# Kernel tuning notes

Hardware: AMD Instinct MI355X
Metric: run time of the kernel (lower is better)

Reference implementation:

```python
import jax, jax.numpy as jnp
import numpy as np

NUM_HEADS = 3
DIM = 96
MLP_HIDDEN = int(DIM * 4.0)
LN_EPS = 1e-5


def _layernorm(x, g, b):
    mu = jnp.mean(x, axis=-1, keepdims=True)
    var = jnp.mean(jnp.square(x - mu), axis=-1, keepdims=True)
    return (x - mu) * jax.lax.rsqrt(var + LN_EPS) * g + b


def setup_inputs() -> dict:
    key = jax.random.key(0)
    ks = jax.random.split(key, 12)
    B, H, W, T, C = 1, 48, 48, 48, DIM
    L = H * W * T
    s = 0.02
    return {
        "x": jax.random.normal(ks[0], (B, L, C), dtype=jnp.float32),
        "mask_matrix": jnp.zeros((1, 1), dtype=jnp.float32),
        "ln1_g": jnp.ones((C,), jnp.float32),
        "ln1_b": jnp.zeros((C,), jnp.float32),
        "qkv_w": jax.random.normal(ks[1], (3 * C, C), jnp.float32) * s,
        "qkv_b": jnp.zeros((3 * C,), jnp.float32),
        "proj_w": jax.random.normal(ks[2], (C, C), jnp.float32) * s,
        "proj_b": jnp.zeros((C,), jnp.float32),
        "ln2_g": jnp.ones((C,), jnp.float32),
        "ln2_b": jnp.zeros((C,), jnp.float32),
        "fc1_w": jax.random.normal(ks[3], (MLP_HIDDEN, C), jnp.float32) * s,
        "fc1_b": jnp.zeros((MLP_HIDDEN,), jnp.float32),
        "fc2_w": jax.random.normal(ks[4], (C, MLP_HIDDEN), jnp.float32) * s,
        "fc2_b": jnp.zeros((C,), jnp.float32),
        "H": 48, "W": 48, "T": 48,
    }


def reference(x, mask_matrix, ln1_g, ln1_b, qkv_w, qkv_b, proj_w, proj_b,
              ln2_g, ln2_b, fc1_w, fc1_b, fc2_w, fc2_b, H, W, T):
    B, L, C = x.shape
    nh = NUM_HEADS
    hd = C // nh
    scale = hd ** -0.5

    shortcut = x
    h = _layernorm(x, ln1_g, ln1_b)
    # [B,H,W,T,C] -> permute(0,3,1,2,4) -> [B*T, H*W, C]  (axial_dims='12', extra_dim=3)
    h = h.reshape(B, H, W, T, C).transpose(0, 3, 1, 2, 4).reshape(B * T, H * W, C)
    B_, N, _ = h.shape

    qkv = h @ qkv_w.T + qkv_b                       # [B_, N, 3C]
    # faithful to torch: permute(1,0,2) -> reshape(1,N,3,nh,B_*hd) -> permute(2,0,3,1,4)
    qkv = jnp.transpose(qkv, (1, 0, 2)).reshape(1, N, 3, nh, B_ * hd)
    qkv = jnp.transpose(qkv, (2, 0, 3, 1, 4))       # [3, 1, nh, N, B_*hd]
    q, k, v = qkv[0] * scale, qkv[1], qkv[2]

    attn = jax.nn.softmax(q @ jnp.swapaxes(k, -2, -1), axis=-1)  # [1, nh, N, N]
    o = attn @ v                                    # [1, nh, N, B_*hd]
    o = jnp.transpose(o, (0, 2, 1, 3)).reshape(B_, N, C)
    o = o @ proj_w.T + proj_b
    # faithful to torch: plain view back to [B, H*W*T, C] (no inverse permute)
    o = o.reshape(B, H * W * T, C)

    x = shortcut + o
    h2 = _layernorm(x, ln2_g, ln2_b)
    m = jax.nn.gelu(h2 @ fc1_w.T + fc1_b, approximate=False) @ fc2_w.T + fc2_b
    return x + m
```

## Files before the change

kernel.cpp:

```cpp
#include <hip/hip_runtime.h>
#include <hip/hip_bf16.h>
#include <math.h>

typedef __bf16 bf16_t;
typedef __bf16 bf16x8 __attribute__((ext_vector_type(8)));
typedef __bf16 bf16x4 __attribute__((ext_vector_type(4)));
typedef float f32x4 __attribute__((ext_vector_type(4)));

#define AS1q __attribute__((address_space(1)))
#define AS3q __attribute__((address_space(3)))

__device__ __forceinline__ void gload_lds16(const bf16_t* g, bf16_t* l) {
    __builtin_amdgcn_global_load_lds((AS1q void*)g, (AS3q void*)l, 16, 0, 0);
}

#define LROWS   110592
#define CDIM    96
#define NTOK    2304
#define FDIM    1536
#define YSTR    3538944ll
#define SSTR    5308416ll
#define SCALE_Q 0.1767766952966369f

__global__ __launch_bounds__(256)
void conv_w(const float* __restrict__ a, const float* __restrict__ b,
            const float* __restrict__ c, const float* __restrict__ d,
            bf16_t* __restrict__ out)
{
    int i = blockIdx.x * 256 + threadIdx.x;
    float v;
    if (i < 27648)       v = a[i];
    else if (i < 36864)  v = b[i - 27648];
    else if (i < 73728)  v = c[i - 36864];
    else                 v = d[i - 73728];
    out[i] = (bf16_t)v;
}

__global__ __launch_bounds__(256)
void ln4_kernel(const float* __restrict__ x, const float* __restrict__ gamma,
                const float* __restrict__ beta, bf16_t* __restrict__ out, int permute)
{
    int wave = threadIdx.x >> 6;
    int half = (threadIdx.x >> 5) & 1;
    int cl   = threadIdx.x & 31;
    int row  = blockIdx.x * 8 + wave * 2 + half;
    bool act = cl < 24;
    const f32x4* xr = (const f32x4*)(x + (size_t)row * CDIM);
    f32x4 v = {0.f, 0.f, 0.f, 0.f};
    if (act) v = xr[cl];
    float s = v[0] + v[1] + v[2] + v[3];
    #pragma unroll
    for (int off = 16; off > 0; off >>= 1) s += __shfl_xor(s, off, 64);
    float mean = s * (1.f / 96.f);
    f32x4 d = {0.f, 0.f, 0.f, 0.f};
    if (act) { d[0]=v[0]-mean; d[1]=v[1]-mean; d[2]=v[2]-mean; d[3]=v[3]-mean; }
    float vs = d[0]*d[0] + d[1]*d[1] + d[2]*d[2] + d[3]*d[3];
    #pragma unroll
    for (int off = 16; off > 0; off >>= 1) vs += __shfl_xor(vs, off, 64);
    float rstd = rsqrtf(vs * (1.f / 96.f) + 1e-5f);
    size_t orow = row;
    if (permute) { int t = row % 48; int n = row / 48; orow = (size_t)t * NTOK + n; }
    if (act) {
        f32x4 g = ((const f32x4*)gamma)[cl];
        f32x4 b = ((const f32x4*)beta)[cl];
        bf16x4 o;
        #pragma unroll
        for (int j = 0; j < 4; j++) o[j] = (bf16_t)(d[j] * rstd * g[j] + b[j]);
        *(bf16x4*)(out + orow * CDIM + cl * 4) = o;
    }
}

__global__ __launch_bounds__(256)
void transpose_v(const bf16_t* __restrict__ Y, bf16_t* __restrict__ Yv)
{
    __shared__ bf16_t tile[64][65];
    const bf16_t* src = Y + (size_t)(6 + blockIdx.z) * YSTR;
    bf16_t* dst = Yv + (size_t)blockIdx.z * YSTR;
    int m0 = blockIdx.x * 64, n0 = blockIdx.y * 64;
    int nl = threadIdx.x >> 2, ch = threadIdx.x & 3;
    const bf16x8* s8 = (const bf16x8*)(src + (size_t)(n0 + nl) * FDIM + m0 + ch * 16);
    bf16x8 va = s8[0], vb = s8[1];
    #pragma unroll
    for (int j = 0; j < 8; j++) tile[nl][ch * 16 + j] = va[j];
    #pragma unroll
    for (int j = 0; j < 8; j++) tile[nl][ch * 16 + 8 + j] = vb[j];
    __syncthreads();
    bf16_t* d = dst + (size_t)(m0 + nl) * NTOK + n0 + ch * 16;
    #pragma unroll
    for (int j = 0; j < 16; j++) d[j] = tile[ch * 16 + j][nl];
}

__global__ __launch_bounds__(256)
void softmax_k(const float* __restrict__ S, bf16_t* __restrict__ P,
               long long sZ, long long pZ)
{
    __shared__ float red[8];
    const float* sr = S + (size_t)blockIdx.z * sZ + (size_t)blockIdx.x * NTOK;
    bf16_t* pr = P + (size_t)blockIdx.z * pZ + (size_t)blockIdx.x * NTOK;
    int wave = threadIdx.x >> 6, lane = threadIdx.x & 63;
    float v[9];
    float mx = -1e30f;
    #pragma unroll
    for (int t = 0; t < 9; t++) { v[t] = sr[t * 256 + threadIdx.x]; mx = fmaxf(mx, v[t]); }
    for (int off = 32; off > 0; off >>= 1) mx = fmaxf(mx, __shfl_xor(mx, off, 64));
    if (lane == 0) red[wave] = mx;
    __syncthreads();
    mx = fmaxf(fmaxf(red[0], red[1]), fmaxf(red[2], red[3]));
    float sum = 0.f;
    #pragma unroll
    for (int t = 0; t < 9; t++) { v[t] = __expf(v[t] - mx); sum += v[t]; }
    for (int off = 32; off > 0; off >>= 1) sum += __shfl_xor(sum, off, 64);
    if (lane == 0) red[4 + wave] = sum;
    __syncthreads();
    sum = red[4] + red[5] + red[6] + red[7];
    float inv = 1.f / sum;
    #pragma unroll
    for (int t = 0; t < 9; t++) pr[t * 256 + threadIdx.x] = (bf16_t)(v[t] * inv);
}

template<int BN, int EPI, int NBY>
__global__ __launch_bounds__(256, 2)
void gemm_bt(const bf16_t* __restrict__ A, const bf16_t* __restrict__ W,
             void* __restrict__ out, int K,
             long long aZ, long long wZ, long long oZ, float scale)
{
    constexpr int BM = 128, BK = 64;
    constexpr int MI = 4;
    constexpr int NT = BN / 32;
    constexpr int NB = 18 * NBY;
    constexpr int CHK = (NB + 7) / 8;
    __shared__ bf16_t As[BM * BK];
    __shared__ bf16_t Bs[BN * BK];

    int id = blockIdx.x;
    int id2 = (id & 7) * CHK + (id >> 3);
    if (id2 >= NB) return;
    int p  = id2 / 108;
    int r_ = id2 - p * 108;
    int by = p * 6 + (r_ % 6);
    int bx = r_ / 6;

    const int tid = threadIdx.x;
    const int wave = tid >> 6, lane = tid & 63;
    const int quad = lane >> 4, l16 = lane & 15;
    const int wm = wave & 1, wn = wave >> 1;
    const int z = blockIdx.z;
    A += (size_t)z * aZ;
    W += (size_t)z * wZ;
    const int m0 = bx * BM, n0 = by * BN;

    f32x4 acc[MI][NT];
    #pragma unroll
    for (int i = 0; i < MI; i++)
        #pragma unroll
        for (int j = 0; j < NT; j++) { f32x4 zz = {0.f, 0.f, 0.f, 0.f}; acc[i][j] = zz; }

    const int srow = lane >> 3;
    const int scol = lane & 7;

    for (int k0 = 0; k0 < K; k0 += BK) {
        __syncthreads();
        for (int it = wave; it < BM / 8; it += 4) {
            int r = it * 8 + srow;
            int cg = scol ^ (r & 7);
            gload_lds16(A + (size_t)(m0 + r) * K + k0 + cg * 8, &As[it * 512]);
        }
        for (int it = wave; it < BN / 8; it += 4) {
            int r = it * 8 + srow;
            int cg = scol ^ (r & 7);
            gload_lds16(W + (size_t)(n0 + r) * K + k0 + cg * 8, &Bs[it * 512]);
        }
        __syncthreads();

        bf16x8 af[MI][2], bfr[NT][2];
        #pragma unroll
        for (int i = 0; i < MI; i++) {
            int r = wm * 64 + i * 16 + l16;
            #pragma unroll
            for (int kk = 0; kk < 2; kk++)
                af[i][kk] = *(const bf16x8*)&As[r * 64 + (((kk * 4 + quad) ^ (r & 7)) << 3)];
        }
        #pragma unroll
        for (int j = 0; j < NT; j++) {
            int c = wn * (BN / 2) + j * 16 + l16;
            #pragma unroll
            for (int kk = 0; kk < 2; kk++)
                bfr[j][kk] = *(const bf16x8*)&Bs[c * 64 + (((kk * 4 + quad) ^ (c & 7)) << 3)];
        }
        #pragma unroll
        for (int kk = 0; kk < 2; kk++)
            #pragma unroll
            for (int i = 0; i < MI; i++)
                #pragma unroll
                for (int j = 0; j < NT; j++)
                    acc[i][j] = __builtin_amdgcn_mfma_f32_16x16x32_bf16(af[i][kk], bfr[j][kk], acc[i][j], 0, 0, 0);
    }

    #pragma unroll
    for (int i = 0; i < MI; i++)
        #pragma unroll
        for (int j = 0; j < NT; j++)
            #pragma unroll
            for (int ri = 0; ri < 4; ri++) {
                int r = m0 + wm * 64 + i * 16 + quad * 4 + ri;
                int c = n0 + wn * (BN / 2) + j * 16 + l16;
                float v = acc[i][j][ri];
                if constexpr (EPI == 1) {
                    float* op = (float*)out + (size_t)z * oZ;
                    op[(size_t)r * NTOK + c] = v * scale;
                } else {
                    int b = r / 48, rr = r - b * 48;
                    ((bf16_t*)out)[((size_t)(b * NTOK + rr * 48 + z * 16)) * CDIM + c] = (bf16_t)v;
                }
            }
}

template<int N, int K, int KC, int EPI>
__global__ __launch_bounds__(256, 2)
void gemm_ws(const bf16_t* __restrict__ A, const bf16_t* __restrict__ Wg,
             void* __restrict__ out, const float* __restrict__ bias,
             const float* __restrict__ resid,
             bf16_t* __restrict__ out2, const float* __restrict__ g2,
             const float* __restrict__ b2)
{
    constexpr int KP = K + 8;
    constexpr int NT = N / 16;
    constexpr int KI = KC / 32;
    __shared__ __attribute__((aligned(16))) bf16_t Ws[N * KP];

    const int tid = threadIdx.x;
    const int wave = tid >> 6, lane = tid & 63;
    const int quad = lane >> 4, l16 = lane & 15;
    const int m0 = blockIdx.x * 256;

    constexpr int CH = N * K / 8;
    for (int c = tid; c < CH; c += 256) {
        int row = c / (K / 8), kc = c - row * (K / 8);
        bf16x8 w = *(const bf16x8*)(Wg + row * K + kc * 8);
        *(bf16x8*)(Ws + row * KP + kc * 8) = w;
    }
    __syncthreads();

    const bf16_t* Ar = A + (size_t)(m0 + wave * 64 + l16) * K + quad * 8;

    const int t = m0 / NTOK;
    const int nb = m0 - t * NTOK;

    auto epi_tile = [&](int nt, const f32x4* a4) {
        int c = nt * 16 + l16;
        if constexpr (EPI == 0) {
            int jj = t * 288 + c;
            int g = jj / FDIM, mm = jj - g * FDIM;
            float bv = bias[c];
            bf16_t* yp = (bf16_t*)out + (size_t)g * YSTR + mm;
            #pragma unroll
            for (int i = 0; i < 4; i++)
                #pragma unroll
                for (int ri = 0; ri < 4; ri++) {
                    int n = nb + wave * 64 + i * 16 + quad * 4 + ri;
                    yp[(size_t)n * FDIM] = (bf16_t)(a4[i][ri] + bv);
                }
        } else {
            float bv = bias[c];
            #pragma unroll
            for (int i = 0; i < 4; i++)
                #pragma unroll
                for (int ri = 0; ri < 4; ri++) {
                    int r = m0 + wave * 64 + i * 16 + quad * 4 + ri;
                    float v = a4[i][ri] + bv;
                    if constexpr (EPI == 3) {
                        v = 0.5f * v * (1.0f + erff(v * 0.70710678118654752f));
                        ((bf16_t*)out)[(size_t)r * N + c] = (bf16_t)v;
                    } else {
                        ((float*)out)[(size_t)r * N + c] = v + resid[(size_t)r * N + c];
                    }
                }
        }
    };

    if constexpr (KC == K && EPI != 5) {
        bf16x8 af[4][KI];
        #pragma unroll
        for (int i = 0; i < 4; i++)
            #pragma unroll
            for (int kk = 0; kk < KI; kk++)
                af[i][kk] = *(const bf16x8*)(Ar + (size_t)i * 16 * K + kk * 32);
        #pragma unroll 2
        for (int nt = 0; nt < NT; nt++) {
            bf16x8 bfr[KI];
            #pragma unroll
            for (int kk = 0; kk < KI; kk++)
                bfr[kk] = *(const bf16x8*)(Ws + (nt * 16 + l16) * KP + kk * 32 + quad * 8);
            f32x4 a4[4];
            #pragma unroll
            for (int i = 0; i < 4; i++) { f32x4 zz = {0.f, 0.f, 0.f, 0.f}; a4[i] = zz; }
            #pragma unroll
            for (int kk = 0; kk < KI; kk++)
                #pragma unroll
                for (int i = 0; i < 4; i++)
                    a4[i] = __builtin_amdgcn_mfma_f32_16x16x32_bf16(af[i][kk], bfr[kk], a4[i], 0, 0, 0);
            epi_tile(nt, a4);
        }
    } else {
        f32x4 acc[4][NT];
        #pragma unroll
        for (int i = 0; i < 4; i++)
            #pragma unroll
            for (int j = 0; j < NT; j++) { f32x4 zz = {0.f, 0.f, 0.f, 0.f}; acc[i][j] = zz; }
        for (int kc0 = 0; kc0 < K; kc0 += KC) {
            bf16x8 af[4][KI];
            #pragma unroll
            for (int i = 0; i < 4; i++)
                #pragma unroll
                for (int kk = 0; kk < KI; kk++)
                    af[i][kk] = *(const bf16x8*)(Ar + (size_t)i * 16 * K + kc0 + kk * 32);
            #pragma unroll
            for (int nt = 0; nt < NT; nt++) {
                #pragma unroll
                for (int kk = 0; kk < KI; kk++) {
                    bf16x8 b = *(const bf16x8*)(Ws + (nt * 16 + l16) * KP + kc0 + kk * 32 + quad * 8);
                    #pragma unroll
                    for (int i = 0; i < 4; i++)
                        acc[i][nt] = __builtin_amdgcn_mfma_f32_16x16x32_bf16(af[i][kk], b, acc[i][nt], 0, 0, 0);
                }
            }
        }
        if constexpr (EPI == 5) {
            float bv[NT], gv[NT], bb[NT];
            #pragma unroll
            for (int nt = 0; nt < NT; nt++) {
                int c = nt * 16 + l16;
                bv[nt] = bias[c]; gv[nt] = g2[c]; bb[nt] = b2[c];
            }
            #pragma unroll
            for (int i = 0; i < 4; i++)
                #pragma unroll
                for (int ri = 0; ri < 4; ri++) {
                    int r = m0 + wave * 64 + i * 16 + quad * 4 + ri;
                    float u[NT];
                    float s = 0.f;
                    #pragma unroll
                    for (int nt = 0; nt < NT; nt++) {
                        int c = nt * 16 + l16;
                        u[nt] = acc[i][nt][ri] + bv[nt] + resid[(size_t)r * N + c];
                        ((float*)out)[(size_t)r * N + c] = u[nt];
                        s += u[nt];
                    }
                    #pragma unroll
                    for (int off = 8; off > 0; off >>= 1) s += __shfl_xor(s, off, 64);
                    float mean = s * (1.f / 96.f);
                    float vs = 0.f;
                    #pragma unroll
                    for (int nt = 0; nt < NT; nt++) {
                        float dd = u[nt] - mean;
                        u[nt] = dd;
                        vs += dd * dd;
                    }
                    #pragma unroll
                    for (int off = 8; off > 0; off >>= 1) vs += __shfl_xor(vs, off, 64);
                    float rstd = rsqrtf(vs * (1.f / 96.f) + 1e-5f);
                    #pragma unroll
                    for (int nt = 0; nt < NT; nt++) {
                        int c = nt * 16 + l16;
                        out2[(size_t)r * N + c] = (bf16_t)(u[nt] * rstd * gv[nt] + bb[nt]);
                    }
                }
        } else {
            #pragma unroll
            for (int nt = 0; nt < NT; nt++) {
                f32x4 a4[4];
                #pragma unroll
                for (int i = 0; i < 4; i++) a4[i] = acc[i][nt];
                epi_tile(nt, a4);
            }
        }
    }
}

extern "C" void kernel_launch(void* const* d_in, const int* in_sizes, int n_in,
                              void* d_out, int out_size, void* d_ws, size_t ws_size,
                              hipStream_t stream)
{
    const float* x      = (const float*)d_in[0];
    const float* ln1_g  = (const float*)d_in[2];
    const float* ln1_b  = (const float*)d_in[3];
    const float* qkv_w  = (const float*)d_in[4];
    const float* qkv_b  = (const float*)d_in[5];
    const float* proj_w = (const float*)d_in[6];
    const float* proj_b = (const float*)d_in[7];
    const float* ln2_g  = (const float*)d_in[8];
    const float* ln2_b  = (const float*)d_in[9];
    const float* fc1_w  = (const float*)d_in[10];
    const float* fc1_b  = (const float*)d_in[11];
    const float* fc2_w  = (const float*)d_in[12];
    const float* fc2_b  = (const float*)d_in[13];

    const size_t SZ_WB = 110592ull * 2;
    const size_t SZ_HP = 10616832ull * 2;
    const size_t SZ_Y  = 31850496ull * 2;
    const size_t SZ_YV = 10616832ull * 2;

    char* ws = (char*)d_ws;
    size_t oWB = 0;
    size_t oHP = oWB + SZ_WB;
    size_t oY  = oHP + SZ_HP;
    size_t oYV = oY + SZ_Y;
    size_t oS  = oYV + SZ_YV;

    bf16_t* Wb    = (bf16_t*)(ws + oWB);
    bf16_t* Wqkv  = Wb;
    bf16_t* Wproj = Wb + 27648;
    bf16_t* Wfc1  = Wb + 36864;
    bf16_t* Wfc2  = Wb + 73728;
    bf16_t* hp    = (bf16_t*)(ws + oHP);
    bf16_t* Y     = (bf16_t*)(ws + oY);
    bf16_t* Yv    = (bf16_t*)(ws + oYV);
    bf16_t* Pb    = (bf16_t*)(ws + oY);
    bf16_t* t1    = (bf16_t*)(ws + oY);
    float*  Sb    = (float*)(ws + oS);
    float*  x2    = (float*)(ws + oS);
    float*  outp  = (float*)d_out;

    dim3 blk(256);

    conv_w<<<dim3(432), blk, 0, stream>>>(qkv_w, proj_w, fc1_w, fc2_w, Wb);
    ln4_kernel<<<dim3(13824), blk, 0, stream>>>(x, ln1_g, ln1_b, hp, 1);
    gemm_ws<288, 96, 96, 0><<<dim3(432), blk, 0, stream>>>(hp, Wqkv, Y, qkv_b,
                                                           nullptr, nullptr, nullptr, nullptr);
    transpose_v<<<dim3(24, 36, 3), blk, 0, stream>>>(Y, Yv);

    gemm_bt<128, 1, 18><<<dim3(328, 1, 3), blk, 0, stream>>>(Y, Y + 3 * YSTR, Sb,
                                                             1536, YSTR, YSTR, SSTR, SCALE_Q);
    softmax_k<<<dim3(2304, 1, 3), blk, 0, stream>>>(Sb, Pb, SSTR, SSTR);
    gemm_bt<128, 2, 12><<<dim3(216, 1, 3), blk, 0, stream>>>(Pb, Yv, hp,
                                                             2304, SSTR, YSTR, 0, 0.f);

    gemm_ws<96, 96, 96, 5><<<dim3(432), blk, 0, stream>>>(hp, Wproj, x2, proj_b, x,
                                                          hp, ln2_g, ln2_b);
    gemm_ws<384, 96, 96, 3><<<dim3(432), blk, 0, stream>>>(hp, Wfc1, t1, fc1_b,
                                                           nullptr, nullptr, nullptr, nullptr);
    gemm_ws<96, 384, 96, 4><<<dim3(432), blk, 0, stream>>>(t1, Wfc2, outp, fc2_b, x2,
                                                           nullptr, nullptr, nullptr);
}
```

Before: 403.6 us.

## Fuse MLP, store scores in bf16, write V transposed from QKV epilogue

```diff
diff --git a/kernel.cpp b/kernel.cpp
--- a/kernel.cpp
+++ b/kernel.cpp
@@ -71,51 +71,36 @@
 }
 
 __global__ __launch_bounds__(256)
-void transpose_v(const bf16_t* __restrict__ Y, bf16_t* __restrict__ Yv)
-{
-    __shared__ bf16_t tile[64][65];
-    const bf16_t* src = Y + (size_t)(6 + blockIdx.z) * YSTR;
-    bf16_t* dst = Yv + (size_t)blockIdx.z * YSTR;
-    int m0 = blockIdx.x * 64, n0 = blockIdx.y * 64;
-    int nl = threadIdx.x >> 2, ch = threadIdx.x & 3;
-    const bf16x8* s8 = (const bf16x8*)(src + (size_t)(n0 + nl) * FDIM + m0 + ch * 16);
-    bf16x8 va = s8[0], vb = s8[1];
-    #pragma unroll
-    for (int j = 0; j < 8; j++) tile[nl][ch * 16 + j] = va[j];
-    #pragma unroll
-    for (int j = 0; j < 8; j++) tile[nl][ch * 16 + 8 + j] = vb[j];
-    __syncthreads();
-    bf16_t* d = dst + (size_t)(m0 + nl) * NTOK + n0 + ch * 16;
-    #pragma unroll
-    for (int j = 0; j < 16; j++) d[j] = tile[ch * 16 + j][nl];
-}
-
-__global__ __launch_bounds__(256)
-void softmax_k(const float* __restrict__ S, bf16_t* __restrict__ P,
+void softmax_k(const bf16_t* __restrict__ S, bf16_t* __restrict__ P,
                long long sZ, long long pZ)
 {
-    __shared__ float red[8];
-    const float* sr = S + (size_t)blockIdx.z * sZ + (size_t)blockIdx.x * NTOK;
-    bf16_t* pr = P + (size_t)blockIdx.z * pZ + (size_t)blockIdx.x * NTOK;
-    int wave = threadIdx.x >> 6, lane = threadIdx.x & 63;
-    float v[9];
+    int wv = threadIdx.x >> 6, lane = threadIdx.x & 63;
+    int row = blockIdx.x * 4 + wv;
+    const bf16_t* sr = S + (size_t)blockIdx.z * sZ + (size_t)row * NTOK;
+    bf16_t* pr = P + (size_t)blockIdx.z * pZ + (size_t)row * NTOK;
+    float v[36];
     float mx = -1e30f;
     #pragma unroll
-    for (int t = 0; t < 9; t++) { v[t] = sr[t * 256 + threadIdx.x]; mx = fmaxf(mx, v[t]); }
+    for (int t = 0; t < 9; t++) {
+        bf16x4 c = *(const bf16x4*)(sr + (size_t)(t * 64 + lane) * 4);
+        #pragma unroll
+        for (int j = 0; j < 4; j++) { v[t*4+j] = (float)c[j]; mx = fmaxf(mx, v[t*4+j]); }
+    }
+    #pragma unroll
     for (int off = 32; off > 0; off >>= 1) mx = fmaxf(mx, __shfl_xor(mx, off, 64));
-    if (lane == 0) red[wave] = mx;
-    __syncthreads();
-    mx = fmaxf(fmaxf(red[0], red[1]), fmaxf(red[2], red[3]));
     float sum = 0.f;
     #pragma unroll
-    for (int t = 0; t < 9; t++) { v[t] = __expf(v[t] - mx); sum += v[t]; }
+    for (int j = 0; j < 36; j++) { v[j] = __expf(v[j] - mx); sum += v[j]; }
+    #pragma unroll
     for (int off = 32; off > 0; off >>= 1) sum += __shfl_xor(sum, off, 64);
-    if (lane == 0) red[4 + wave] = sum;
-    __syncthreads();
-    sum = red[4] + red[5] + red[6] + red[7];
     float inv = 1.f / sum;
     #pragma unroll
-    for (int t = 0; t < 9; t++) pr[t * 256 + threadIdx.x] = (bf16_t)(v[t] * inv);
+    for (int t = 0; t < 9; t++) {
+        bf16x4 o;
+        #pragma unroll
+        for (int j = 0; j < 4; j++) o[j] = (bf16_t)(v[t*4+j] * inv);
+        *(bf16x4*)(pr + (size_t)(t * 64 + lane) * 4) = o;
+    }
 }
 
 template<int BN, int EPI, int NBY>
@@ -206,8 +191,8 @@
                 int c = n0 + wn * (BN / 2) + j * 16 + l16;
                 float v = acc[i][j][ri];
                 if constexpr (EPI == 1) {
-                    float* op = (float*)out + (size_t)z * oZ;
-                    op[(size_t)r * NTOK + c] = v * scale;
+                    bf16_t* op = (bf16_t*)out + (size_t)z * oZ;
+                    op[(size_t)r * NTOK + c] = (bf16_t)(v * scale);
                 } else {
                     int b = r / 48, rr = r - b * 48;
                     ((bf16_t*)out)[((size_t)(b * NTOK + rr * 48 + z * 16)) * CDIM + c] = (bf16_t)v;
@@ -252,14 +237,26 @@
             int jj = t * 288 + c;
             int g = jj / FDIM, mm = jj - g * FDIM;
             float bv = bias[c];
-            bf16_t* yp = (bf16_t*)out + (size_t)g * YSTR + mm;
-            #pragma unroll
-            for (int i = 0; i < 4; i++)
-                #pragma unroll
-                for (int ri = 0; ri < 4; ri++) {
-                    int n = nb + wave * 64 + i * 16 + quad * 4 + ri;
-                    yp[(size_t)n * FDIM] = (bf16_t)(a4[i][ri] + bv);
+            if (g < 6) {
+                bf16_t* yp = (bf16_t*)out + (size_t)g * YSTR + mm;
+                #pragma unroll
+                for (int i = 0; i < 4; i++)
+                    #pragma unroll
+                    for (int ri = 0; ri < 4; ri++) {
+                        int n = nb + wave * 64 + i * 16 + quad * 4 + ri;
+                        yp[(size_t)n * FDIM] = (bf16_t)(a4[i][ri] + bv);
+                    }
+            } else {
+                bf16_t* vp = out2 + (size_t)(g - 6) * YSTR + (size_t)mm * NTOK;
+                #pragma unroll
+                for (int i = 0; i < 4; i++) {
+                    int n0q = nb + wave * 64 + i * 16 + quad * 4;
+                    bf16x4 o;
+                    #pragma unroll
+                    for (int ri = 0; ri < 4; ri++) o[ri] = (bf16_t)(a4[i][ri] + bv);
+                    *(bf16x4*)(vp + n0q) = o;
                 }
+            }
         } else {
             float bv = bias[c];
             #pragma unroll
@@ -375,6 +372,114 @@
             }
         }
     }
+}
+
+__global__ __launch_bounds__(256, 1)
+void mlp_fused(const bf16_t* __restrict__ A, const bf16_t* __restrict__ W1g,
+               const bf16_t* __restrict__ W2g, const float* __restrict__ b1,
+               const float* __restrict__ b2, const float* __restrict__ resid,
+               float* __restrict__ out)
+{
+    constexpr int KP1 = 104;
+    __shared__ __attribute__((aligned(16))) bf16_t W1s[384 * KP1];
+    __shared__ __attribute__((aligned(16))) bf16_t W2c[96 * 40];
+    __shared__ __attribute__((aligned(16))) bf16_t Tb[256 * 40];
+
+    const int tid = threadIdx.x;
+    const int wave = tid >> 6, lane = tid & 63;
+    const int quad = lane >> 4, l16 = lane & 15;
+    const int m0 = blockIdx.x * 256;
+
+    for (int c = tid; c < 384 * 12; c += 256) {
+        int row = c / 12, kc = c - row * 12;
+        bf16x8 w = *(const bf16x8*)(W1g + row * 96 + kc * 8);
+        *(bf16x8*)(W1s + row * KP1 + kc * 8) = w;
+    }
+
+    const bf16_t* Ar = A + (size_t)(m0 + wave * 64 + l16) * 96 + quad * 8;
+    bf16x8 af[4][3];
+    #pragma unroll
+    for (int i = 0; i < 4; i++)
+        #pragma unroll
+        for (int kk = 0; kk < 3; kk++)
+            af[i][kk] = *(const bf16x8*)(Ar + (size_t)i * 16 * 96 + kk * 32);
+
+    __syncthreads();
+
+    f32x4 acc2[4][6];
+    #pragma unroll
+    for (int i = 0; i < 4; i++)
+        #pragma unroll
+        for (int j = 0; j < 6; j++) { f32x4 zz = {0.f, 0.f, 0.f, 0.f}; acc2[i][j] = zz; }
+
+    for (int c = 0; c < 12; c++) {
+        bf16x4 w2r[3];
+        #pragma unroll
+        for (int q = 0; q < 3; q++) {
+            int e = q * 256 + tid;
+            int row = e >> 3, sub = e & 7;
+            w2r[q] = *(const bf16x4*)(W2g + row * 384 + c * 32 + sub * 4);
+        }
+        f32x4 a1[4][2];
+        #pragma unroll
+        for (int i = 0; i < 4; i++)
+            #pragma unroll
+            for (int s = 0; s < 2; s++) { f32x4 zz = {0.f, 0.f, 0.f, 0.f}; a1[i][s] = zz; }
+        #pragma unroll
+        for (int s = 0; s < 2; s++) {
+            int n = c * 32 + s * 16 + l16;
+            #pragma unroll
+            for (int kk = 0; kk < 3; kk++) {
+                bf16x8 b = *(const bf16x8*)(W1s + n * KP1 + kk * 32 + quad * 8);
+                #pragma unroll
+                for (int i = 0; i < 4; i++)
+                    a1[i][s] = __builtin_amdgcn_mfma_f32_16x16x32_bf16(af[i][kk], b, a1[i][s], 0, 0, 0);
+            }
+        }
+        __syncthreads();
+        #pragma unroll
+        for (int s = 0; s < 2; s++) {
+            int n = c * 32 + s * 16 + l16;
+            float bv = b1[n];
+            #pragma unroll
+            for (int i = 0; i < 4; i++)
+                #pragma unroll
+                for (int ri = 0; ri < 4; ri++) {
+                    float u = a1[i][s][ri] + bv;
+                    u = 0.5f * u * (1.0f + erff(u * 0.70710678118654752f));
+                    Tb[(wave * 64 + i * 16 + quad * 4 + ri) * 40 + s * 16 + l16] = (bf16_t)u;
+                }
+        }
+        #pragma unroll
+        for (int q = 0; q < 3; q++) {
+            int e = q * 256 + tid;
+            int row = e >> 3, sub = e & 7;
+            *(bf16x4*)(W2c + row * 40 + sub * 4) = w2r[q];
+        }
+        __syncthreads();
+        bf16x8 a2[4];
+        #pragma unroll
+        for (int i = 0; i < 4; i++)
+            a2[i] = *(const bf16x8*)(Tb + (wave * 64 + i * 16 + l16) * 40 + quad * 8);
+        #pragma unroll
+        for (int nt = 0; nt < 6; nt++) {
+            bf16x8 b = *(const bf16x8*)(W2c + (nt * 16 + l16) * 40 + quad * 8);
+            #pragma unroll
+            for (int i = 0; i < 4; i++)
+                acc2[i][nt] = __builtin_amdgcn_mfma_f32_16x16x32_bf16(a2[i], b, acc2[i][nt], 0, 0, 0);
+        }
+    }
+
+    #pragma unroll
+    for (int i = 0; i < 4; i++)
+        #pragma unroll
+        for (int nt = 0; nt < 6; nt++)
+            #pragma unroll
+            for (int ri = 0; ri < 4; ri++) {
+                int r = m0 + wave * 64 + i * 16 + quad * 4 + ri;
+                int cc = nt * 16 + l16;
+                out[(size_t)r * 96 + cc] = acc2[i][nt][ri] + b2[cc] + resid[(size_t)r * 96 + cc];
+            }
 }
 
 extern "C" void kernel_launch(void* const* d_in, const int* in_sizes, int n_in,
@@ -416,8 +521,7 @@
     bf16_t* Y     = (bf16_t*)(ws + oY);
     bf16_t* Yv    = (bf16_t*)(ws + oYV);
     bf16_t* Pb    = (bf16_t*)(ws + oY);
-    bf16_t* t1    = (bf16_t*)(ws + oY);
-    float*  Sb    = (float*)(ws + oS);
+    bf16_t* Sb    = (bf16_t*)(ws + oS);
     float*  x2    = (float*)(ws + oS);
     float*  outp  = (float*)d_out;
 
@@ -426,19 +530,13 @@
     conv_w<<<dim3(432), blk, 0, stream>>>(qkv_w, proj_w, fc1_w, fc2_w, Wb);
     ln4_kernel<<<dim3(13824), blk, 0, stream>>>(x, ln1_g, ln1_b, hp, 1);
     gemm_ws<288, 96, 96, 0><<<dim3(432), blk, 0, stream>>>(hp, Wqkv, Y, qkv_b,
-                                                           nullptr, nullptr, nullptr, nullptr);
-    transpose_v<<<dim3(24, 36, 3), blk, 0, stream>>>(Y, Yv);
-
+                                                           nullptr, Yv, nullptr, nullptr);
     gemm_bt<128, 1, 18><<<dim3(328, 1, 3), blk, 0, stream>>>(Y, Y + 3 * YSTR, Sb,
                                                              1536, YSTR, YSTR, SSTR, SCALE_Q);
-    softmax_k<<<dim3(2304, 1, 3), blk, 0, stream>>>(Sb, Pb, SSTR, SSTR);
+    softmax_k<<<dim3(576, 1, 3), blk, 0, stream>>>(Sb, Pb, SSTR, SSTR);
     gemm_bt<128, 2, 12><<<dim3(216, 1, 3), blk, 0, stream>>>(Pb, Yv, hp,
                                                              2304, SSTR, YSTR, 0, 0.f);
-
     gemm_ws<96, 96, 96, 5><<<dim3(432), blk, 0, stream>>>(hp, Wproj, x2, proj_b, x,
                                                           hp, ln2_g, ln2_b);
-    gemm_ws<384, 96, 96, 3><<<dim3(432), blk, 0, stream>>>(hp, Wfc1, t1, fc1_b,
-                                                           nullptr, nullptr, nullptr, nullptr);
-    gemm_ws<96, 384, 96, 4><<<dim3(432), blk, 0, stream>>>(t1, Wfc2, outp, fc2_b, x2,
-                                                           nullptr, nullptr, nullptr);
-}
+    mlp_fused<<<dim3(432), blk, 0, stream>>>(hp, Wfc1, Wfc2, fc1_b, fc2_b, x2, outp);
+}
```

Measured after the change: 393.2 us. 2.6% less time.
